# Performance work log

Hardware: AMD Instinct MI355X
Metric: run time of the kernel (lower is better)

The kernel has to match this reference:

```python
import jax, jax.numpy as jnp
import numpy as np

N_LENGTH = 64
MAX_NUM_FRAME = 16
EPS = 1e-6  # torch pairwise_distance eps


def setup_inputs() -> dict:
    key = jax.random.key(0)
    x = jax.random.normal(key, (8, N_LENGTH, 3, 224, 224), dtype=jnp.float32)
    # frozen conv params per init_parameters(): weight=0.001, bias=0
    conv_w = jnp.full((1, 3, 7, 7), 0.001, dtype=jnp.float32)
    conv_b = jnp.zeros((1,), dtype=jnp.float32)
    return {"x": x, "conv_w": conv_w, "conv_b": conv_b}


def reference(x, conv_w, conv_b):
    B, L, C, H, W = x.shape
    xc = x.reshape(B * L, C, H, W)
    # shallow_conv: 3->1 channels, 7x7, stride 1, pad 3
    y = jax.lax.conv_general_dilated(
        xc, conv_w, window_strides=(1, 1), padding=[(3, 3), (3, 3)],
        dimension_numbers=("NCHW", "OIHW", "NCHW"))
    y = y + conv_b[None, :, None, None]
    y = y.reshape(B, L, H * W)  # out channels == 1, flattened spatially

    # PairwiseDistance(p=2) over the singleton channel dim: |a - b + eps|
    pa = jnp.abs(y[:, :-1, :] - y[:, 1:, :] + EPS)  # (B, L-1, H*W)

    diff_score = pa.sum(axis=-1)  # (B, L-1) == PA.sum(dim=(-2,-1))
    ratio = MAX_NUM_FRAME / N_LENGTH
    dsp = jnp.power(diff_score, ratio ** 0.5)
    frac = dsp / dsp.sum(axis=-1, keepdims=True)
    # einsum('bl,ml->bml', frac, tril_ones).sum(-1) is a cumsum along l
    cum = jnp.cumsum(frac, axis=-1)  # (B, L-1)

    interval = 1.0 / (MAX_NUM_FRAME - 1)
    sample = jnp.arange(MAX_NUM_FRAME, dtype=jnp.float32) * interval  # (M,)
    # vectorized argmin over all M sample points at once
    idx = jnp.argmin(jnp.abs(cum[:, None, :] - sample[None, :, None]), axis=-1)  # (B, M)

    sel = jnp.take_along_axis(x, idx[:, :, None, None, None], axis=1)  # (B, M, 3, H, W)
    return sel
```

## Files before the change

kernel.cpp:

```cpp
#include <hip/hip_runtime.h>
#include <float.h>
#include <math.h>

#define HH 224
#define WW 224
#define PLANE (HH*WW)
#define FRAME (3*HH*WW)
#define LFR 64
#define NP 63
#define NB 8
#define NM 16
#define EPSV 1e-6f

#define RSLAB 32
#define NSLAB (HH / RSLAB)
#define DROWS (RSLAB + 6)
#define LDW 232
#define NQ 56
#define UNITS (DROWS * NQ)

__global__ __launch_bounds__(256) void diff_kernel(
    const float* __restrict__ x, const float* __restrict__ cw,
    float* __restrict__ dsp)
{
    const int slab = blockIdx.x;
    const int pair = blockIdx.y;
    const int b = pair / NP;
    const int l = pair - b * NP;
    const float* f0 = x + (size_t)(b * LFR + l) * FRAME;
    const float* f1 = f0 + FRAME;
    const float w = cw[0];

    const int rBase = slab * RSLAB - 3;

    __shared__ float Dl[DROWS][LDW];
    __shared__ float red[4];

    const int tid = threadIdx.x;

    if (tid < 2 * DROWS) {
        const int r = tid >> 1;
        const int col = (tid & 1) ? (LDW - 4) : 0;
        *(float4*)&Dl[r][col] = make_float4(0.f, 0.f, 0.f, 0.f);
    }

    for (int u = tid; u < UNITS; u += 256) {
        const int r  = u / NQ;
        const int cq = u - r * NQ;
        const int gr = rBase + r;
        float4 v = make_float4(0.f, 0.f, 0.f, 0.f);
        if (gr >= 0 && gr < HH) {
            const int off = (gr * WW + cq * 4) >> 2;
            const float4* p0 = (const float4*)f0;
            const float4* p1 = (const float4*)f1;
            const float4 a0 = p0[off];
            const float4 a1 = p0[off + PLANE/4];
            const float4 a2 = p0[off + 2*PLANE/4];
            const float4 b0 = p1[off];
            const float4 b1 = p1[off + PLANE/4];
            const float4 b2 = p1[off + 2*PLANE/4];
            v.x = (a0.x - b0.x) + (a1.x - b1.x) + (a2.x - b2.x);
            v.y = (a0.y - b0.y) + (a1.y - b1.y) + (a2.y - b2.y);
            v.z = (a0.z - b0.z) + (a1.z - b1.z) + (a2.z - b2.z);
            v.w = (a0.w - b0.w) + (a1.w - b1.w) + (a2.w - b2.w);
        }
        *(float4*)&Dl[r][4 + cq * 4] = v;
    }
    __syncthreads();

    float acc = 0.f;
    if (tid < WW) {
        const int base = 4 + tid;
        float hring[8];
        #pragma unroll
        for (int r = 0; r < DROWS; ++r) {
            float h = 0.f;
            #pragma unroll
            for (int k = 0; k < 7; ++k) h += Dl[r][base - 3 + k];
            hring[r & 7] = h;
            if (r >= 6) {
                float v = 0.f;
                #pragma unroll
                for (int k = 0; k < 7; ++k) v += hring[(r - 6 + k) & 7];
                acc += fabsf(w * v + EPSV);
            }
        }
    }

    #pragma unroll
    for (int off = 32; off >= 1; off >>= 1)
        acc += __shfl_down(acc, off, 64);
    const int wave = tid >> 6;
    if ((tid & 63) == 0) red[wave] = acc;
    __syncthreads();
    if (tid == 0)
        dsp[pair * NSLAB + slab] = red[0] + red[1] + red[2] + red[3];
}

__global__ __launch_bounds__(64) void select_kernel(
    const float* __restrict__ dsp, int* __restrict__ idx)
{
    const int b = blockIdx.x;
    const int lane = threadIdx.x;
    float v = 0.f;
    if (lane < NP) {
        float s = 0.f;
        #pragma unroll
        for (int k = 0; k < NSLAB; ++k) s += dsp[(b * NP + lane) * NSLAB + k];
        v = sqrtf(s);
    }

    float tot = v;
    #pragma unroll
    for (int off = 1; off < 64; off <<= 1)
        tot += __shfl_xor(tot, off, 64);

    float scan = v;
    #pragma unroll
    for (int off = 1; off < 64; off <<= 1) {
        float t = __shfl_up(scan, off, 64);
        if (lane >= off) scan += t;
    }
    const float cum = scan / tot;

    const float interval = 1.0f / (NM - 1);
    for (int m = 0; m < NM; ++m) {
        const float target = (float)m * interval;
        float bv = (lane < NP) ? fabsf(cum - target) : FLT_MAX;
        int bi = lane;
        #pragma unroll
        for (int off = 1; off < 64; off <<= 1) {
            float ov = __shfl_xor(bv, off, 64);
            int oi = __shfl_xor(bi, off, 64);
            if (ov < bv || (ov == bv && oi < bi)) { bv = ov; bi = oi; }
        }
        if (lane == 0) idx[b * NM + m] = bi;
    }
}

__global__ __launch_bounds__(256) void gather_kernel(
    const float* __restrict__ x, const int* __restrict__ idx,
    float* __restrict__ out)
{
    const int f = blockIdx.y;
    const int b = f >> 4;
    const int id = idx[f];
    const float4* src = (const float4*)(x + (size_t)(b * LFR + id) * FRAME);
    float4* dst = (float4*)(out + (size_t)f * FRAME);
    const int i = blockIdx.x * 256 + threadIdx.x;
    #pragma unroll
    for (int k = 0; k < 7; ++k)
        dst[i + k * (21 * 256)] = src[i + k * (21 * 256)];
}

extern "C" void kernel_launch(void* const* d_in, const int* in_sizes, int n_in,
                              void* d_out, int out_size, void* d_ws, size_t ws_size,
                              hipStream_t stream) {
    const float* x  = (const float*)d_in[0];
    const float* cw = (const float*)d_in[1];
    float* dsp = (float*)d_ws;
    int*   idx = (int*)((char*)d_ws + 16384);

    hipLaunchKernelGGL(diff_kernel, dim3(NSLAB, NB * NP), dim3(256), 0, stream,
                       x, cw, dsp);
    hipLaunchKernelGGL(select_kernel, dim3(NB), dim3(64), 0, stream, dsp, idx);
    hipLaunchKernelGGL(gather_kernel, dim3(21, NB * NM), dim3(256), 0, stream,
                       x, idx, (float*)d_out);
}
```

Before: 467.2 us.

## Reuse per-frame conv results across consecutive pairs in diff kernel

Result: slower. 496.7 us (+6.3%).

```diff
diff --git a/kernel.cpp b/kernel.cpp
--- a/kernel.cpp
+++ b/kernel.cpp
@@ -17,24 +17,26 @@
 #define DROWS (RSLAB + 6)
 #define LDW 232
 #define NQ 56
-#define UNITS (DROWS * NQ)
+#define UNITS3 (DROWS * NQ)
+#define KP 7
+#define NG (NP / KP)
+#define FPB (KP + 1)
 
 __global__ __launch_bounds__(256) void diff_kernel(
     const float* __restrict__ x, const float* __restrict__ cw,
     float* __restrict__ dsp)
 {
     const int slab = blockIdx.x;
-    const int pair = blockIdx.y;
-    const int b = pair / NP;
-    const int l = pair - b * NP;
-    const float* f0 = x + (size_t)(b * LFR + l) * FRAME;
-    const float* f1 = f0 + FRAME;
-    const float w = cw[0];
+    const int bg   = blockIdx.y;
+    const int b    = bg / NG;
+    const int g    = bg - b * NG;
+    const int l0   = g * KP;
+    const float w  = cw[0];
 
     const int rBase = slab * RSLAB - 3;
 
     __shared__ float Dl[DROWS][LDW];
-    __shared__ float red[4];
+    __shared__ float red[KP][4];
 
     const int tid = threadIdx.x;
 
@@ -44,57 +46,61 @@
         *(float4*)&Dl[r][col] = make_float4(0.f, 0.f, 0.f, 0.f);
     }
 
-    for (int u = tid; u < UNITS; u += 256) {
-        const int r  = u / NQ;
-        const int cq = u - r * NQ;
-        const int gr = rBase + r;
-        float4 v = make_float4(0.f, 0.f, 0.f, 0.f);
-        if (gr >= 0 && gr < HH) {
-            const int off = (gr * WW + cq * 4) >> 2;
-            const float4* p0 = (const float4*)f0;
-            const float4* p1 = (const float4*)f1;
-            const float4 a0 = p0[off];
-            const float4 a1 = p0[off + PLANE/4];
-            const float4 a2 = p0[off + 2*PLANE/4];
-            const float4 b0 = p1[off];
-            const float4 b1 = p1[off + PLANE/4];
-            const float4 b2 = p1[off + 2*PLANE/4];
-            v.x = (a0.x - b0.x) + (a1.x - b1.x) + (a2.x - b2.x);
-            v.y = (a0.y - b0.y) + (a1.y - b1.y) + (a2.y - b2.y);
-            v.z = (a0.z - b0.z) + (a1.z - b1.z) + (a2.z - b2.z);
-            v.w = (a0.w - b0.w) + (a1.w - b1.w) + (a2.w - b2.w);
+    float Wprev[RSLAB];
+
+    #pragma unroll 1
+    for (int f = 0; f < FPB; ++f) {
+        const float4* p = (const float4*)(x + (size_t)(b * LFR + l0 + f) * FRAME);
+        for (int u = tid; u < UNITS3; u += 256) {
+            const int r  = u / NQ;
+            const int cq = u - r * NQ;
+            const int gr = rBase + r;
+            float4 v = make_float4(0.f, 0.f, 0.f, 0.f);
+            if (gr >= 0 && gr < HH) {
+                const int off = (gr * WW + cq * 4) >> 2;
+                const float4 a0 = p[off];
+                const float4 a1 = p[off + PLANE/4];
+                const float4 a2 = p[off + 2*PLANE/4];
+                v.x = a0.x + a1.x + a2.x;
+                v.y = a0.y + a1.y + a2.y;
+                v.z = a0.z + a1.z + a2.z;
+                v.w = a0.w + a1.w + a2.w;
+            }
+            *(float4*)&Dl[r][4 + cq * 4] = v;
         }
-        *(float4*)&Dl[r][4 + cq * 4] = v;
-    }
-    __syncthreads();
+        __syncthreads();
 
-    float acc = 0.f;
-    if (tid < WW) {
-        const int base = 4 + tid;
-        float hring[8];
-        #pragma unroll
-        for (int r = 0; r < DROWS; ++r) {
-            float h = 0.f;
+        float pacc = 0.f;
+        if (tid < WW) {
+            float Hrow[DROWS];
             #pragma unroll
-            for (int k = 0; k < 7; ++k) h += Dl[r][base - 3 + k];
-            hring[r & 7] = h;
-            if (r >= 6) {
-                float v = 0.f;
+            for (int r = 0; r < DROWS; ++r) {
+                float h = Dl[r][tid + 1];
                 #pragma unroll
-                for (int k = 0; k < 7; ++k) v += hring[(r - 6 + k) & 7];
-                acc += fabsf(w * v + EPSV);
+                for (int k = 2; k <= 7; ++k) h += Dl[r][tid + k];
+                Hrow[r] = h;
+            }
+            #pragma unroll
+            for (int i = 0; i < RSLAB; ++i) {
+                const float Wc = Hrow[i] + Hrow[i+1] + Hrow[i+2] + Hrow[i+3]
+                               + Hrow[i+4] + Hrow[i+5] + Hrow[i+6];
+                if (f > 0) pacc += fabsf(w * (Wprev[i] - Wc) + EPSV);
+                Wprev[i] = Wc;
             }
         }
+        if (f > 0) {
+            #pragma unroll
+            for (int off = 32; off >= 1; off >>= 1)
+                pacc += __shfl_down(pacc, off, 64);
+            if ((tid & 63) == 0) red[f - 1][tid >> 6] = pacc;
+        }
+        __syncthreads();
     }
 
-    #pragma unroll
-    for (int off = 32; off >= 1; off >>= 1)
-        acc += __shfl_down(acc, off, 64);
-    const int wave = tid >> 6;
-    if ((tid & 63) == 0) red[wave] = acc;
-    __syncthreads();
-    if (tid == 0)
-        dsp[pair * NSLAB + slab] = red[0] + red[1] + red[2] + red[3];
+    if (tid < KP) {
+        dsp[(b * NP + l0 + tid) * NSLAB + slab] =
+            red[tid][0] + red[tid][1] + red[tid][2] + red[tid][3];
+    }
 }
 
 __global__ __launch_bounds__(64) void select_kernel(
@@ -161,7 +167,7 @@
     float* dsp = (float*)d_ws;
     int*   idx = (int*)((char*)d_ws + 16384);
 
-    hipLaunchKernelGGL(diff_kernel, dim3(NSLAB, NB * NP), dim3(256), 0, stream,
+    hipLaunchKernelGGL(diff_kernel, dim3(NSLAB, NB * NG), dim3(256), 0, stream,
                        x, cw, dsp);
     hipLaunchKernelGGL(select_kernel, dim3(NB), dim3(64), 0, stream, dsp, idx);
     hipLaunchKernelGGL(gather_kernel, dim3(21, NB * NM), dim3(256), 0, stream,
```
